# Optimization experiments

Hardware: AMD Instinct MI355X
Metric: run time of the kernel (lower is better)

## Reference

```python
import jax, jax.numpy as jnp
import numpy as np
import math

B, C, H, W = 8, 512, 32, 32
NUM_GROUPS = 32
NUM_HEADS = C // 64  # num_head_channels=64 -> 8 heads
EPS = 1e-5


def setup_inputs() -> dict:
    key = jax.random.key(0)
    ks = jax.random.split(key, 7)
    x = jax.random.normal(ks[0], (B, C, H, W), dtype=jnp.float32)
    gn_w = jax.random.uniform(ks[1], (C,), dtype=jnp.float32, minval=0.5, maxval=1.5)
    gn_b = jax.random.normal(ks[2], (C,), dtype=jnp.float32) * 0.1
    qkv_w = jax.random.normal(ks[3], (3 * C, C), dtype=jnp.float32) * 0.02
    qkv_b = jax.random.normal(ks[4], (3 * C,), dtype=jnp.float32) * 0.02
    proj_w = jax.random.normal(ks[5], (C, C), dtype=jnp.float32) * 0.02
    proj_b = jax.random.normal(ks[6], (C,), dtype=jnp.float32) * 0.02
    return {"x": x, "gn_w": gn_w, "gn_b": gn_b, "qkv_w": qkv_w,
            "qkv_b": qkv_b, "proj_w": proj_w, "proj_b": proj_b}


def _group_norm(x, w, b):
    # x: [B, C, L]
    bb, cc, ll = x.shape
    g = x.reshape(bb, NUM_GROUPS, cc // NUM_GROUPS, ll)
    mean = g.mean(axis=(2, 3), keepdims=True)
    var = g.var(axis=(2, 3), keepdims=True)
    g = (g - mean) * jax.lax.rsqrt(var + EPS)
    return g.reshape(bb, cc, ll) * w[None, :, None] + b[None, :, None]


def reference(x, gn_w, gn_b, qkv_w, qkv_b, proj_w, proj_b):
    b, c, h, w = x.shape
    L = h * w
    xf = x.reshape(b, c, L)
    # 1x1 conv1d QKV on normalized input: weight [3C, C]
    qkv = jnp.einsum('oc,bcl->bol', qkv_w, _group_norm(xf, gn_w, gn_b)) + qkv_b[None, :, None]
    ch = c // NUM_HEADS  # per-head channels
    qkv = qkv.reshape(b * NUM_HEADS, 3 * ch, L)
    q, k, v = qkv[:, :ch], qkv[:, ch:2 * ch], qkv[:, 2 * ch:]
    scale = 1.0 / math.sqrt(math.sqrt(ch))
    # [b*H, T, S] scores, softmax over source dim (computed in fp32 per source)
    weight = jnp.einsum('bct,bcs->bts', q * scale, k * scale)
    weight = jax.nn.softmax(weight.astype(jnp.float32), axis=-1).astype(weight.dtype)
    a = jnp.einsum('bts,bcs->bct', weight, v).reshape(b, c, L)
    hproj = jnp.einsum('oc,bcl->bol', proj_w, a) + proj_b[None, :, None]
    return (xf + hproj).reshape(b, c, h, w)
```

## Files before the change

### kernel.cpp

```cpp
#include <hip/hip_runtime.h>
#include <math.h>

#define BB 8
#define CC 512
#define LL 1024
#define GG 32
#define CPG 16
#define NH 8
#define CH 64

typedef unsigned short ushort_t;
typedef __attribute__((ext_vector_type(8))) short short8;
typedef __attribute__((ext_vector_type(4))) float f32x4;

#define SCALE_Q 0.18033688f

__device__ inline ushort_t f2bf(float f) {
  union { float f; unsigned u; } v;
  v.f = f;
  unsigned r = v.u + 0x7FFFu + ((v.u >> 16) & 1u);
  return (ushort_t)(r >> 16);
}

__device__ inline unsigned pack_bf2(float lo, float hi) {
  return __builtin_amdgcn_perm(__float_as_uint(hi), __float_as_uint(lo),
                               0x07060302u);
}

__device__ inline int swz(int r, int k) {
  return r * 64 + ((((k >> 3) ^ (r & 7)) << 3) | (k & 7));
}

__device__ __forceinline__ void g2l16(const void* g, void* l) {
  __builtin_amdgcn_global_load_lds((const unsigned int*)g, (unsigned int*)l,
                                   16, 0, 0);
}

__global__ __launch_bounds__(256) void pre_kernel(
    const float* __restrict__ x, const float* __restrict__ gn_w,
    const float* __restrict__ gn_b, const float* __restrict__ qkv_w,
    const float* __restrict__ proj_w, float* __restrict__ s_bc,
    float* __restrict__ t_bc, ushort_t* __restrict__ wq,
    ushort_t* __restrict__ wp) {
  if (blockIdx.x < BB * GG) {
    int b = blockIdx.x / GG;
    int g = blockIdx.x % GG;
    const float4* xg4 =
        (const float4*)(x + ((size_t)b * CC + (size_t)g * CPG) * LL);
    float sum = 0.f, sq = 0.f;
#pragma unroll
    for (int i = 0; i < 16; ++i) {
      float4 v = xg4[threadIdx.x + i * 256];
      sum += (v.x + v.y) + (v.z + v.w);
      sq += (v.x * v.x + v.y * v.y) + (v.z * v.z + v.w * v.w);
    }
#pragma unroll
    for (int off = 32; off > 0; off >>= 1) {
      sum += __shfl_down(sum, off);
      sq += __shfl_down(sq, off);
    }
    __shared__ float red[8];
    __shared__ float st[2];
    int wave = threadIdx.x >> 6;
    if ((threadIdx.x & 63) == 0) {
      red[wave] = sum;
      red[4 + wave] = sq;
    }
    __syncthreads();
    if (threadIdx.x == 0) {
      float s = red[0] + red[1] + red[2] + red[3];
      float q = red[4] + red[5] + red[6] + red[7];
      float mean = s * (1.f / (CPG * LL));
      float var = q * (1.f / (CPG * LL)) - mean * mean;
      st[0] = mean;
      st[1] = rsqrtf(var + 1e-5f);
    }
    __syncthreads();
    if (threadIdx.x < CPG) {
      int c = g * CPG + threadIdx.x;
      float w = gn_w[c];
      float sc = st[1] * w;
      s_bc[b * CC + c] = sc;
      t_bc[b * CC + c] = gn_b[c] - st[0] * sc;
    }
  } else {
    int cb = blockIdx.x - BB * GG;
    int idx = (cb * 256 + threadIdx.x) * 4;
    const int N1 = 3 * CC * CC;
    float4 v;
    ushort_t* mat;
    int row, k;
    if (idx < N1) {
      v = *(const float4*)(qkv_w + idx);
      row = idx >> 9;
      k = idx & 511;
      mat = wq + (size_t)row * CC;
    } else {
      int j = idx - N1;
      v = *(const float4*)(proj_w + j);
      row = j >> 9;
      k = j & 511;
      mat = wp + (size_t)row * CC;
    }
    int dcol = (k & ~63) | ((((k >> 3) & 7) ^ (row & 7)) << 3) | (k & 7);
    unsigned lo = f2bf(v.x) | ((unsigned)f2bf(v.y) << 16);
    unsigned hi = f2bf(v.z) | ((unsigned)f2bf(v.w) << 16);
    *(uint2*)(mat + dcol) = make_uint2(lo, hi);
  }
}

__global__ __launch_bounds__(256) void xnt_kernel(
    const float* __restrict__ x, const float* __restrict__ s_bc,
    const float* __restrict__ t_bc, ushort_t* __restrict__ xnT) {
  const int b = blockIdx.z;
  const int c0 = blockIdx.y * 64;
  const int l0 = blockIdx.x * 64;
  const int tid = threadIdx.x;
  __shared__ ushort_t Ts[64 * 72];
#pragma unroll
  for (int r4 = 0; r4 < 4; ++r4) {
    int c_local = (tid >> 4) + r4 * 16;
    int l_local = (tid & 15) * 4;
    int c = c0 + c_local;
    float sc = s_bc[b * CC + c], sh = t_bc[b * CC + c];
    float4 v = *(const float4*)(x + ((size_t)b * CC + c) * LL + l0 + l_local);
    float vv[4] = {v.x, v.y, v.z, v.w};
#pragma unroll
    for (int dl = 0; dl < 4; ++dl) {
      int l = l_local + dl;
      int cs = c_local ^ (((l >> 2) & 7) << 3);
      Ts[l * 72 + cs] = f2bf(vv[dl] * sc + sh);
    }
  }
  __syncthreads();
#pragma unroll
  for (int rep = 0; rep < 2; ++rep) {
    int gid = tid + rep * 256;
    int l = gid >> 3, seg = gid & 7;
    uint4 v = *(const uint4*)&Ts[l * 72 + ((seg * 8) ^ (((l >> 2) & 7) << 3))];
    *(uint4*)(xnT + ((size_t)b * LL + l0 + l) * CC + c0 +
              ((seg ^ (l & 7)) << 3)) = v;
  }
}

__global__ __launch_bounds__(256) void qkv_mfma_kernel(
    const ushort_t* __restrict__ wq, const ushort_t* __restrict__ xnT,
    const float* __restrict__ qkv_b, ushort_t* __restrict__ qT,
    ushort_t* __restrict__ kT, ushort_t* __restrict__ vbuf) {
  const int b = blockIdx.z;
  const int m0 = blockIdx.y * 128;
  const int n0 = blockIdx.x * 128;
  const int tid = threadIdx.x;
  const int w = tid >> 6, lane = tid & 63;
  const int col = lane & 15, quad = lane >> 4;
  const int wm = (w >> 1) * 64, wn = (w & 1) * 64;
  __shared__ ushort_t Smem[2 * 128 * 64];
  ushort_t* As = Smem;
  ushort_t* Bs = Smem + 128 * 64;
  f32x4 acc[4][4];
  f32x4 z = {0.f, 0.f, 0.f, 0.f};
#pragma unroll
  for (int i = 0; i < 4; ++i)
#pragma unroll
    for (int j = 0; j < 4; ++j) acc[i][j] = z;

  const ushort_t* arow = wq + (size_t)m0 * CC;
  const ushort_t* brow = xnT + ((size_t)b * LL + n0) * CC;
  const int eb = w * 2048 + lane * 8;

  for (int k0 = 0; k0 < CC; k0 += 64) {
    __syncthreads();
#pragma unroll
    for (int i = 0; i < 4; ++i) {
      int ee = eb + i * 512;
      int r = ee >> 6, c = ee & 63;
      g2l16(arow + (size_t)r * CC + k0 + c, As + (w * 2048 + i * 512));
      g2l16(brow + (size_t)r * CC + k0 + c, Bs + (w * 2048 + i * 512));
    }
    __syncthreads();
#pragma unroll
    for (int kk = 0; kk < 2; ++kk) {
      short8 af[4], bf[4];
#pragma unroll
      for (int mi = 0; mi < 4; ++mi)
        af[mi] = *(const short8*)&As[swz(wm + mi * 16 + col, kk * 32 + quad * 8)];
#pragma unroll
      for (int ni = 0; ni < 4; ++ni)
        bf[ni] = *(const short8*)&Bs[swz(wn + ni * 16 + col, kk * 32 + quad * 8)];
#pragma unroll
      for (int mi = 0; mi < 4; ++mi)
#pragma unroll
        for (int ni = 0; ni < 4; ++ni)
          acc[mi][ni] = __builtin_amdgcn_mfma_f32_16x16x32_bf16(
              af[mi], bf[ni], acc[mi][ni], 0, 0, 0);
    }
  }
  __syncthreads();
  const int chunk_g = (m0 >> 6) + (w >> 1);
  const int sel = chunk_g % 3;
  ushort_t* Tile = Smem + (w >> 1) * 8192;
  if (sel < 2) {
    const float sc = (sel == 0) ? SCALE_Q : 1.f;
#pragma unroll
    for (int mi = 0; mi < 4; ++mi) {
      int mg = m0 + wm + mi * 16 + quad * 4;
      float b0 = qkv_b[mg + 0], b1 = qkv_b[mg + 1];
      float b2 = qkv_b[mg + 2], b3 = qkv_b[mg + 3];
      int ch = mi * 16 + quad * 4;
#pragma unroll
      for (int ni = 0; ni < 4; ++ni) {
        int lloc = wn + ni * 16 + col;
        float v0 = (acc[mi][ni][0] + b0) * sc;
        float v1 = (acc[mi][ni][1] + b1) * sc;
        float v2 = (acc[mi][ni][2] + b2) * sc;
        float v3 = (acc[mi][ni][3] + b3) * sc;
        int chs = ch ^ ((lloc & 7) << 3);
        *(uint2*)&Tile[lloc * 64 + chs] =
            make_uint2(pack_bf2(v0, v1), pack_bf2(v2, v3));
      }
    }
  } else {
#pragma unroll
    for (int mi = 0; mi < 4; ++mi)
#pragma unroll
      for (int r = 0; r < 4; ++r) {
        int ch = mi * 16 + quad * 4 + r;
        float bias = qkv_b[m0 + wm + ch];
#pragma unroll
        for (int ni = 0; ni < 4; ++ni) {
          int lloc = wn + ni * 16 + col;
          Tile[ch * 128 + lloc] =
              (ushort_t)(__float_as_uint(acc[mi][ni][r] + bias) >> 16);
        }
      }
  }
  __syncthreads();
#pragma unroll
  for (int ci = 0; ci < 2; ++ci) {
    int cg = (m0 >> 6) + ci;
    int head = cg / 3, sel2 = cg % 3;
    int bh = b * NH + head;
    ushort_t* T2 = Smem + ci * 8192;
    if (sel2 < 2) {
      ushort_t* dst = (sel2 == 0) ? qT : kT;
#pragma unroll
      for (int it = 0; it < 4; ++it) {
        int idx = tid + it * 256;
        int l = idx >> 3, seg = idx & 7;
        uint4 v = *(const uint4*)&T2[l * 64 + seg * 8];
        *(uint4*)(dst + ((size_t)bh * LL + n0 + l) * CC / 8 * 0 +
                  ((size_t)bh * LL + n0 + l) * CH + seg * 8) = v;
      }
    } else {
#pragma unroll
      for (int it = 0; it < 4; ++it) {
        int idx = tid + it * 256;
        int ch = idx >> 4, lseg = idx & 15;
        uint4 v = *(const uint4*)&T2[ch * 128 + lseg * 8];
        int g = lseg & 7, blk = lseg >> 3;
        *(uint4*)(vbuf + ((size_t)bh * CH + ch) * LL + n0 + blk * 64 +
                  ((g ^ (ch & 7)) << 3)) = v;
      }
    }
  }
}

__global__ __launch_bounds__(256) void attn_mfma_kernel(
    const ushort_t* __restrict__ qT, const ushort_t* __restrict__ kT,
    const ushort_t* __restrict__ vbuf, ushort_t* __restrict__ abuf) {
  const int Bx = blockIdx.x;
  const int bh = (Bx & 7) * 8 + ((Bx >> 3) >> 4);
  const int t0g = ((Bx >> 3) & 15) * 64;
  const int b = bh >> 3, h = bh & 7;
  const int tid = threadIdx.x;
  const int w = tid >> 6, lane = tid & 63;
  const int col = lane & 15, quad = lane >> 4;
  const int strip = w * 16;
  __shared__ ushort_t Ps[64 * 64];
  __shared__ ushort_t Ksm[2][64 * 64];
  __shared__ ushort_t Vsm[2][64 * 64];

  const ushort_t* kbase = kT + (size_t)bh * LL * CH;
  const ushort_t* vbase = vbuf + (size_t)bh * CH * LL;
  const int eb = w * 1024 + lane * 8;

#pragma unroll
  for (int i = 0; i < 2; ++i) {
    int ee = eb + i * 512;
    g2l16(kbase + ee, &Ksm[0][w * 1024 + i * 512]);
    g2l16(vbase + (size_t)(ee >> 6) * LL + (ee & 63),
          &Vsm[0][w * 1024 + i * 512]);
  }
  const ushort_t* qtile = qT + ((size_t)bh * LL + t0g) * CH;
  short8 bq[2];
  bq[0] = *(const short8*)&qtile[swz(strip + col, quad * 8)];
  bq[1] = *(const short8*)&qtile[swz(strip + col, 32 + quad * 8)];

  float m_s = 0.f, lsum = 0.f;
  f32x4 oacc[4];
  f32x4 z = {0.f, 0.f, 0.f, 0.f};
#pragma unroll
  for (int ci = 0; ci < 4; ++ci) oacc[ci] = z;
  __syncthreads();

  int cur = 0;
  for (int it = 0; it < 16; ++it) {
    if (it < 15) {
      const ushort_t* kn = kbase + (size_t)(it + 1) * 64 * CH;
      const ushort_t* vn = vbase + (it + 1) * 64;
#pragma unroll
      for (int i = 0; i < 2; ++i) {
        int ee = eb + i * 512;
        g2l16(kn + ee, &Ksm[cur ^ 1][w * 1024 + i * 512]);
        g2l16(vn + (size_t)(ee >> 6) * LL + (ee & 63),
              &Vsm[cur ^ 1][w * 1024 + i * 512]);
      }
    }
    const ushort_t* Kc = Ksm[cur];
    const ushort_t* Vc = Vsm[cur];
    f32x4 sacc[4];
#pragma unroll
    for (int si = 0; si < 4; ++si) sacc[si] = z;
    __builtin_amdgcn_s_setprio(1);
#pragma unroll
    for (int kk = 0; kk < 2; ++kk)
#pragma unroll
      for (int si = 0; si < 4; ++si) {
        short8 ak = *(const short8*)&Kc[swz(si * 16 + col, kk * 32 + quad * 8)];
        sacc[si] = __builtin_amdgcn_mfma_f32_16x16x32_bf16(ak, bq[kk],
                                                           sacc[si], 0, 0, 0);
      }
    __builtin_amdgcn_s_setprio(0);
    if (it == 0) {
      float mx = sacc[0][0];
#pragma unroll
      for (int si = 0; si < 4; ++si)
#pragma unroll
        for (int r = 0; r < 4; ++r) mx = fmaxf(mx, sacc[si][r]);
      mx = fmaxf(mx, __shfl_xor(mx, 16));
      mx = fmaxf(mx, __shfl_xor(mx, 32));
      m_s = mx;
    }
#pragma unroll
    for (int si = 0; si < 4; ++si) {
      float p0 = __builtin_amdgcn_exp2f(sacc[si][0] - m_s);
      float p1 = __builtin_amdgcn_exp2f(sacc[si][1] - m_s);
      float p2 = __builtin_amdgcn_exp2f(sacc[si][2] - m_s);
      float p3 = __builtin_amdgcn_exp2f(sacc[si][3] - m_s);
      lsum += (p0 + p1) + (p2 + p3);
      int base = swz(strip + col, si * 16 + quad * 4);
      *(unsigned*)&Ps[base] = pack_bf2(p0, p1);
      *(unsigned*)&Ps[base + 2] = pack_bf2(p2, p3);
    }
    __builtin_amdgcn_s_setprio(1);
#pragma unroll
    for (int kk = 0; kk < 2; ++kk) {
      short8 ap = *(const short8*)&Ps[swz(strip + col, kk * 32 + quad * 8)];
#pragma unroll
      for (int ci = 0; ci < 4; ++ci) {
        short8 bv = *(const short8*)&Vc[swz(ci * 16 + col, kk * 32 + quad * 8)];
        oacc[ci] = __builtin_amdgcn_mfma_f32_16x16x32_bf16(ap, bv, oacc[ci],
                                                           0, 0, 0);
      }
    }
    __builtin_amdgcn_s_setprio(0);
    __syncthreads();
    cur ^= 1;
  }
  lsum += __shfl_xor(lsum, 16);
  lsum += __shfl_xor(lsum, 32);
  float linv[4];
#pragma unroll
  for (int r = 0; r < 4; ++r)
    linv[r] = 1.f / __shfl(lsum, (lane & 48) | (quad * 4 + r), 64);
#pragma unroll
  for (int r = 0; r < 4; ++r) {
    int l = t0g + strip + quad * 4 + r;
#pragma unroll
    for (int ci = 0; ci < 4; ++ci) {
      int cl = ci * 16 + col;
      int dcol = ((((cl >> 3) ^ (l & 7)) << 3) | (cl & 7));
      abuf[((size_t)b * LL + l) * CC + h * CH + dcol] =
          f2bf(oacc[ci][r] * linv[r]);
    }
  }
}

__global__ __launch_bounds__(256) void proj_mfma_kernel(
    const ushort_t* __restrict__ wp, const ushort_t* __restrict__ abuf,
    const float* __restrict__ proj_b, const float* __restrict__ x,
    float* __restrict__ out) {
  const int b = blockIdx.z;
  const int m0 = blockIdx.y * 64;
  const int n0 = blockIdx.x * 128;
  const int tid = threadIdx.x;
  const int w = tid >> 6, lane = tid & 63;
  const int col = lane & 15, quad = lane >> 4;
  const int wm = (w >> 1) * 32, wn = (w & 1) * 64;
  __shared__ ushort_t As[64 * 64];
  __shared__ ushort_t Bs[128 * 64];
  f32x4 acc[2][4];
  f32x4 z = {0.f, 0.f, 0.f, 0.f};
#pragma unroll
  for (int i = 0; i < 2; ++i)
#pragma unroll
    for (int j = 0; j < 4; ++j) acc[i][j] = z;

  const ushort_t* arow = wp + (size_t)m0 * CC;
  const ushort_t* brow = abuf + ((size_t)b * LL + n0) * CC;
  const int ea = w * 1024 + lane * 8;
  const int ebb = w * 2048 + lane * 8;

  for (int k0 = 0; k0 < CC; k0 += 64) {
    __syncthreads();
#pragma unroll
    for (int i = 0; i < 2; ++i) {
      int ee = ea + i * 512;
      g2l16(arow + (size_t)(ee >> 6) * CC + k0 + (ee & 63),
            As + (w * 1024 + i * 512));
    }
#pragma unroll
    for (int i = 0; i < 4; ++i) {
      int ee = ebb + i * 512;
      g2l16(brow + (size_t)(ee >> 6) * CC + k0 + (ee & 63),
            Bs + (w * 2048 + i * 512));
    }
    __syncthreads();
#pragma unroll
    for (int kk = 0; kk < 2; ++kk) {
      short8 af[2], bf[4];
#pragma unroll
      for (int mi = 0; mi < 2; ++mi)
        af[mi] = *(const short8*)&As[swz(wm + mi * 16 + col, kk * 32 + quad * 8)];
#pragma unroll
      for (int ni = 0; ni < 4; ++ni)
        bf[ni] = *(const short8*)&Bs[swz(wn + ni * 16 + col, kk * 32 + quad * 8)];
#pragma unroll
      for (int mi = 0; mi < 2; ++mi)
#pragma unroll
        for (int ni = 0; ni < 4; ++ni)
          acc[mi][ni] = __builtin_amdgcn_mfma_f32_16x16x32_bf16(
              af[mi], bf[ni], acc[mi][ni], 0, 0, 0);
    }
  }
#pragma unroll
  for (int mi = 0; mi < 2; ++mi)
#pragma unroll
    for (int r = 0; r < 4; ++r) {
      int o = m0 + wm + mi * 16 + quad * 4 + r;
      float bias = proj_b[o];
#pragma unroll
      for (int ni = 0; ni < 4; ++ni) {
        int l = n0 + wn + ni * 16 + col;
        size_t off = ((size_t)b * CC + o) * LL + l;
        out[off] = x[off] + bias + acc[mi][ni][r];
      }
    }
}

extern "C" void kernel_launch(void* const* d_in, const int* in_sizes, int n_in,
                              void* d_out, int out_size, void* d_ws,
                              size_t ws_size, hipStream_t stream) {
  const float* x = (const float*)d_in[0];
  const float* gn_w = (const float*)d_in[1];
  const float* gn_b = (const float*)d_in[2];
  const float* qkv_w = (const float*)d_in[3];
  const float* qkv_b = (const float*)d_in[4];
  const float* proj_w = (const float*)d_in[5];
  const float* proj_b = (const float*)d_in[6];
  float* out = (float*)d_out;

  char* ws = (char*)d_ws;
  float* s_bc = (float*)ws;
  float* t_bc = s_bc + BB * CC;
  ushort_t* wq = (ushort_t*)(t_bc + BB * CC);
  ushort_t* wp = wq + (size_t)3 * CC * CC;
  ushort_t* xnT = wp + (size_t)CC * CC;
  ushort_t* qT = xnT + (size_t)BB * LL * CC;
  ushort_t* kT = qT + (size_t)BB * NH * LL * CH;
  ushort_t* vb = kT + (size_t)BB * NH * LL * CH;
  ushort_t* abuf = vb + (size_t)BB * NH * LL * CH;

  pre_kernel<<<BB * GG + 1024, 256, 0, stream>>>(x, gn_w, gn_b, qkv_w, proj_w,
                                                 s_bc, t_bc, wq, wp);
  xnt_kernel<<<dim3(LL / 64, CC / 64, BB), 256, 0, stream>>>(x, s_bc, t_bc,
                                                             xnT);
  qkv_mfma_kernel<<<dim3(LL / 128, (3 * CC) / 128, BB), 256, 0, stream>>>(
      wq, xnT, qkv_b, qT, kT, vb);
  attn_mfma_kernel<<<dim3(1024), 256, 0, stream>>>(qT, kT, vb, abuf);
  proj_mfma_kernel<<<dim3(LL / 128, CC / 64, BB), 256, 0, stream>>>(
      wp, abuf, proj_b, x, out);
}
```

Before: 151.1 us.

## Double-buffer LDS in QKV and proj GEMMs; retile QKV to one head per block

Both the QKV and projection GEMM kernels now keep two LDS stages, loading the next K-slice while MFMAs run on the current one, which cuts the main loop to one barrier per step. The QKV kernel also grows to 384 threads and 192-row M tiles, so each block covers exactly one head's q, k and v chunks, which simplifies the epilogue routing. The costs are more LDS per block (80KB for QKV), possibly lower occupancy, and uneven work across waves in the store phase.

```diff
diff --git a/kernel.cpp b/kernel.cpp
--- a/kernel.cpp
+++ b/kernel.cpp
@@ -143,20 +143,18 @@
   }
 }
 
-__global__ __launch_bounds__(256) void qkv_mfma_kernel(
+__global__ __launch_bounds__(384, 3) void qkv_mfma_kernel(
     const ushort_t* __restrict__ wq, const ushort_t* __restrict__ xnT,
     const float* __restrict__ qkv_b, ushort_t* __restrict__ qT,
     ushort_t* __restrict__ kT, ushort_t* __restrict__ vbuf) {
   const int b = blockIdx.z;
-  const int m0 = blockIdx.y * 128;
+  const int m0 = blockIdx.y * 192;
   const int n0 = blockIdx.x * 128;
   const int tid = threadIdx.x;
   const int w = tid >> 6, lane = tid & 63;
   const int col = lane & 15, quad = lane >> 4;
   const int wm = (w >> 1) * 64, wn = (w & 1) * 64;
-  __shared__ ushort_t Smem[2 * 128 * 64];
-  ushort_t* As = Smem;
-  ushort_t* Bs = Smem + 128 * 64;
+  __shared__ ushort_t Smem[2 * 20480];
   f32x4 acc[4][4];
   f32x4 z = {0.f, 0.f, 0.f, 0.f};
 #pragma unroll
@@ -166,18 +164,33 @@
 
   const ushort_t* arow = wq + (size_t)m0 * CC;
   const ushort_t* brow = xnT + ((size_t)b * LL + n0) * CC;
-  const int eb = w * 2048 + lane * 8;
-
-  for (int k0 = 0; k0 < CC; k0 += 64) {
-    __syncthreads();
-#pragma unroll
-    for (int i = 0; i < 4; ++i) {
-      int ee = eb + i * 512;
-      int r = ee >> 6, c = ee & 63;
-      g2l16(arow + (size_t)r * CC + k0 + c, As + (w * 2048 + i * 512));
-      g2l16(brow + (size_t)r * CC + k0 + c, Bs + (w * 2048 + i * 512));
-    }
-    __syncthreads();
+
+  auto stage = [&](int bb, int k0) {
+    ushort_t* As = Smem + bb * 20480;
+    ushort_t* Bs = As + 12288;
+#pragma unroll
+    for (int j = 0; j < 4; ++j) {
+      int e = (j * 6 + w) * 512 + lane * 8;
+      g2l16(arow + (size_t)(e >> 6) * CC + k0 + (e & 63),
+            As + (j * 6 + w) * 512);
+    }
+    if (w < 4) {
+#pragma unroll
+      for (int j = 0; j < 4; ++j) {
+        int e = (j * 4 + w) * 512 + lane * 8;
+        g2l16(brow + (size_t)(e >> 6) * CC + k0 + (e & 63),
+              Bs + (j * 4 + w) * 512);
+      }
+    }
+  };
+
+  stage(0, 0);
+  __syncthreads();
+  int cur = 0;
+  for (int step = 0; step < 8; ++step) {
+    if (step < 7) stage(cur ^ 1, (step + 1) * 64);
+    const ushort_t* As = Smem + cur * 20480;
+    const ushort_t* Bs = As + 12288;
 #pragma unroll
     for (int kk = 0; kk < 2; ++kk) {
       short8 af[4], bf[4];
@@ -194,13 +207,13 @@
           acc[mi][ni] = __builtin_amdgcn_mfma_f32_16x16x32_bf16(
               af[mi], bf[ni], acc[mi][ni], 0, 0, 0);
     }
-  }
-  __syncthreads();
-  const int chunk_g = (m0 >> 6) + (w >> 1);
-  const int sel = chunk_g % 3;
-  ushort_t* Tile = Smem + (w >> 1) * 8192;
-  if (sel < 2) {
-    const float sc = (sel == 0) ? SCALE_Q : 1.f;
+    __syncthreads();
+    cur ^= 1;
+  }
+  const int ci_w = w >> 1;
+  ushort_t* Tile = Smem + ci_w * 8192;
+  if (ci_w < 2) {
+    const float sc = (ci_w == 0) ? SCALE_Q : 1.f;
 #pragma unroll
     for (int mi = 0; mi < 4; ++mi) {
       int mg = m0 + wm + mi * 16 + quad * 4;
@@ -235,31 +248,33 @@
       }
   }
   __syncthreads();
-#pragma unroll
-  for (int ci = 0; ci < 2; ++ci) {
-    int cg = (m0 >> 6) + ci;
-    int head = cg / 3, sel2 = cg % 3;
-    int bh = b * NH + head;
+  const int head = blockIdx.y;
+  const int bh = b * NH + head;
+#pragma unroll
+  for (int ci = 0; ci < 3; ++ci) {
     ushort_t* T2 = Smem + ci * 8192;
-    if (sel2 < 2) {
-      ushort_t* dst = (sel2 == 0) ? qT : kT;
-#pragma unroll
-      for (int it = 0; it < 4; ++it) {
-        int idx = tid + it * 256;
-        int l = idx >> 3, seg = idx & 7;
-        uint4 v = *(const uint4*)&T2[l * 64 + seg * 8];
-        *(uint4*)(dst + ((size_t)bh * LL + n0 + l) * CC / 8 * 0 +
-                  ((size_t)bh * LL + n0 + l) * CH + seg * 8) = v;
+    if (ci < 2) {
+      ushort_t* dst = (ci == 0) ? qT : kT;
+#pragma unroll
+      for (int it = 0; it < 3; ++it) {
+        int idx = tid + it * 384;
+        if (idx < 1024) {
+          int l = idx >> 3, seg = idx & 7;
+          uint4 v = *(const uint4*)&T2[l * 64 + seg * 8];
+          *(uint4*)(dst + ((size_t)bh * LL + n0 + l) * CH + seg * 8) = v;
+        }
       }
     } else {
 #pragma unroll
-      for (int it = 0; it < 4; ++it) {
-        int idx = tid + it * 256;
-        int ch = idx >> 4, lseg = idx & 15;
-        uint4 v = *(const uint4*)&T2[ch * 128 + lseg * 8];
-        int g = lseg & 7, blk = lseg >> 3;
-        *(uint4*)(vbuf + ((size_t)bh * CH + ch) * LL + n0 + blk * 64 +
-                  ((g ^ (ch & 7)) << 3)) = v;
+      for (int it = 0; it < 3; ++it) {
+        int idx = tid + it * 384;
+        if (idx < 1024) {
+          int ch = idx >> 4, lseg = idx & 15;
+          uint4 v = *(const uint4*)&T2[ch * 128 + lseg * 8];
+          int g = lseg & 7, blk = lseg >> 3;
+          *(uint4*)(vbuf + ((size_t)bh * CH + ch) * LL + n0 + blk * 64 +
+                    ((g ^ (ch & 7)) << 3)) = v;
+        }
       }
     }
   }
@@ -397,8 +412,7 @@
   const int w = tid >> 6, lane = tid & 63;
   const int col = lane & 15, quad = lane >> 4;
   const int wm = (w >> 1) * 32, wn = (w & 1) * 64;
-  __shared__ ushort_t As[64 * 64];
-  __shared__ ushort_t Bs[128 * 64];
+  __shared__ ushort_t Smem[2 * 12288];
   f32x4 acc[2][4];
   f32x4 z = {0.f, 0.f, 0.f, 0.f};
 #pragma unroll
@@ -408,24 +422,31 @@
 
   const ushort_t* arow = wp + (size_t)m0 * CC;
   const ushort_t* brow = abuf + ((size_t)b * LL + n0) * CC;
-  const int ea = w * 1024 + lane * 8;
-  const int ebb = w * 2048 + lane * 8;
-
-  for (int k0 = 0; k0 < CC; k0 += 64) {
-    __syncthreads();
-#pragma unroll
-    for (int i = 0; i < 2; ++i) {
-      int ee = ea + i * 512;
-      g2l16(arow + (size_t)(ee >> 6) * CC + k0 + (ee & 63),
-            As + (w * 1024 + i * 512));
-    }
-#pragma unroll
-    for (int i = 0; i < 4; ++i) {
-      int ee = ebb + i * 512;
-      g2l16(brow + (size_t)(ee >> 6) * CC + k0 + (ee & 63),
-            Bs + (w * 2048 + i * 512));
-    }
-    __syncthreads();
+
+  auto stage = [&](int bb, int k0) {
+    ushort_t* As = Smem + bb * 12288;
+    ushort_t* Bs = As + 4096;
+#pragma unroll
+    for (int j = 0; j < 2; ++j) {
+      int e = (j * 4 + w) * 512 + lane * 8;
+      g2l16(arow + (size_t)(e >> 6) * CC + k0 + (e & 63),
+            As + (j * 4 + w) * 512);
+    }
+#pragma unroll
+    for (int j = 0; j < 4; ++j) {
+      int e = (j * 4 + w) * 512 + lane * 8;
+      g2l16(brow + (size_t)(e >> 6) * CC + k0 + (e & 63),
+            Bs + (j * 4 + w) * 512);
+    }
+  };
+
+  stage(0, 0);
+  __syncthreads();
+  int cur = 0;
+  for (int step = 0; step < 8; ++step) {
+    if (step < 7) stage(cur ^ 1, (step + 1) * 64);
+    const ushort_t* As = Smem + cur * 12288;
+    const ushort_t* Bs = As + 4096;
 #pragma unroll
     for (int kk = 0; kk < 2; ++kk) {
       short8 af[2], bf[4];
@@ -442,6 +463,8 @@
           acc[mi][ni] = __builtin_amdgcn_mfma_f32_16x16x32_bf16(
               af[mi], bf[ni], acc[mi][ni], 0, 0, 0);
     }
+    __syncthreads();
+    cur ^= 1;
   }
 #pragma unroll
   for (int mi = 0; mi < 2; ++mi)
@@ -485,7 +508,7 @@
                                                  s_bc, t_bc, wq, wp);
   xnt_kernel<<<dim3(LL / 64, CC / 64, BB), 256, 0, stream>>>(x, s_bc, t_bc,
                                                              xnT);
-  qkv_mfma_kernel<<<dim3(LL / 128, (3 * CC) / 128, BB), 256, 0, stream>>>(
+  qkv_mfma_kernel<<<dim3(LL / 128, 1536 / 192, BB), 384, 0, stream>>>(
       wq, xnT, qkv_b, qT, kT, vb);
   attn_mfma_kernel<<<dim3(1024), 256, 0, stream>>>(qT, kT, vb, abuf);
   proj_mfma_kernel<<<dim3(LL / 128, CC / 64, BB), 256, 0, stream>>>(
```

Measured after the change: 143.9 us. 1.05x faster.
